# Kernel optimization log

Hardware: AMD Instinct MI355X
Metric: run time of the kernel (lower is better)

The kernel has to match this reference:

```python
import jax, jax.numpy as jnp
import numpy as np

# Dimensions implied by init_kwargs: dim=64, shape=(96,64,64), groups=8
DIM = 64          # in_planes = out_planes = conv channel dim (== spatial h == w)
CL = 96           # original channel dim c == attention sequence length
HS = 64           # spatial h (== DIM)
WS = 64           # spatial w (== DIM)
G = 8             # groups
GP = DIM // G     # group_planes = 8
EPS = 1e-5        # BatchNorm eps (inference mode with running stats)
B, T = 2, 16


def _bn(x, gamma, beta, mean, var, axis):
    """BatchNorm in inference mode along `axis`."""
    shp = [1] * x.ndim
    shp[axis] = -1
    return (x - mean.reshape(shp)) * jax.lax.rsqrt(var.reshape(shp) + EPS) * gamma.reshape(shp) + beta.reshape(shp)


def setup_inputs() -> dict:
    key = jax.random.key(0)
    ks = jax.random.split(key, 16)
    inp = {}
    inp["x"] = jax.random.normal(ks[0], (B, T, CL * HS * WS), jnp.float32)
    # qkv_transform: Conv1d(DIM, 2*DIM, kernel=1, bias=False) -> weight (2*DIM, DIM)
    inp["w_qkv"] = jax.random.normal(ks[1], (2 * DIM, DIM), jnp.float32) * np.float32(1.0 / np.sqrt(DIM))
    def bn_params(i, n):
        return (jnp.abs(jax.random.normal(ks[i], (n,), jnp.float32)) * 0.1 + 1.0,
                jax.random.normal(ks[i + 1], (n,), jnp.float32) * 0.1,
                jax.random.normal(ks[i + 2], (n,), jnp.float32) * 0.1,
                jnp.abs(jax.random.normal(ks[i + 3], (n,), jnp.float32)) * 0.1 + 1.0)
    (inp["qkv_gamma"], inp["qkv_beta"], inp["qkv_mean"], inp["qkv_var"]) = bn_params(2, 2 * DIM)
    (inp["sim_gamma"], inp["sim_beta"], inp["sim_mean"], inp["sim_var"]) = bn_params(6, G)
    (inp["out_gamma"], inp["out_beta"], inp["out_mean"], inp["out_var"]) = bn_params(10, DIM)
    return inp


def reference(x, w_qkv, qkv_gamma, qkv_beta, qkv_mean, qkv_var,
              sim_gamma, sim_beta, sim_mean, sim_var,
              out_gamma, out_beta, out_mean, out_var):
    b, t, F = x.shape
    NT = b * t
    xt = x.reshape(NT, CL, HS, WS)              # (NT, c, h, w)
    xt = jnp.transpose(xt, (0, 2, 3, 1))        # permute(0,2,3,1): (NT, h, w, c)
    xf = xt.reshape(NT * HS, WS, CL)            # view(NT*W, H, C): conv batch, channels=WS(=dim), len=c
    # 1x1 Conv1d + BN over channel dim
    qkv = jnp.einsum('oi,bil->bol', w_qkv, xf)  # (B2, 2*DIM, c)
    qkv = _bn(qkv, qkv_gamma, qkv_beta, qkv_mean, qkv_var, axis=1)
    qkv = qkv.reshape(NT * HS, G, 2 * GP, CL)
    q = qkv[:, :, : GP // 2]                    # (B2, G, GP//2, c)
    k = qkv[:, :, GP // 2: GP]                  # (B2, G, GP//2, c)
    v = qkv[:, :, GP:]                          # (B2, G, GP, c)
    qk = jnp.einsum('bgci,bgcj->bgij', q, k)    # (B2, G, c, c)
    qk = _bn(qk, sim_gamma, sim_beta, sim_mean, sim_var, axis=1)
    sim = jax.nn.softmax(qk, axis=3)
    sv = jnp.einsum('bgij,bgcj->bgci', sim, v)  # (B2, G, GP, c)
    sv = sv.reshape(NT * HS, DIM, CL)
    out = _bn(sv, out_gamma, out_beta, out_mean, out_var, axis=1)
    out = out.reshape(NT, HS, DIM, CL)          # (NT, W, out_planes, C); sum over size-1 dim is identity
    out = jnp.transpose(out, (0, 3, 2, 1))      # permute(0,3,2,1): (NT, c, dim, h) == (NT, c, h, w)
    return out.reshape(b, t, F)
```

## Files before the change

### kernel.cpp

```cpp
#include <hip/hip_runtime.h>

#define EPS 1e-5f
#define LOG2E 1.4426950408889634f

typedef short v8s __attribute__((ext_vector_type(8)));
typedef float v4f __attribute__((ext_vector_type(4)));

__device__ inline unsigned cvt_pk_bf16(float a, float b) {
    unsigned r;
    asm("v_cvt_pk_bf16_f32 %0, %1, %2" : "=v"(r) : "v"(a), "v"(b));
    return r;
}
__device__ inline unsigned short f2bf(float f) {
    return (unsigned short)cvt_pk_bf16(f, f);
}
__device__ inline float bf2f(unsigned short u) {
    union { unsigned u; float f; } v; v.u = (unsigned)u << 16;
    return v.f;
}

template<bool DIRECT>
__global__ __launch_bounds__(256, 3) void attn_kernel(
    const float* __restrict__ x,
    const float* __restrict__ w,
    const float* __restrict__ qkv_gamma, const float* __restrict__ qkv_beta,
    const float* __restrict__ qkv_mean,  const float* __restrict__ qkv_var,
    const float* __restrict__ sim_gamma, const float* __restrict__ sim_beta,
    const float* __restrict__ sim_mean,  const float* __restrict__ sim_var,
    const float* __restrict__ out_gamma, const float* __restrict__ out_beta,
    const float* __restrict__ out_mean,  const float* __restrict__ out_var,
    float* __restrict__ dst)
{
    __shared__ __align__(16) unsigned char smem[32256];
    unsigned short (*Qb)[96]  = (unsigned short(*)[96])smem;
    float (*Kf)[96]           = (float(*)[96])(smem + 6144);
    unsigned short (*Vb)[104] = (unsigned short(*)[104])(smem + 18432);
    unsigned short (*Xb)[72]  = (unsigned short(*)[72])smem;
    unsigned short (*Wb)[72]  = (unsigned short(*)[72])(smem + 13824);

    const int tid  = threadIdx.x;
    const int lane = tid & 63;
    const int wid  = tid >> 6;
    const int quad = lane >> 4;
    const int b  = blockIdx.x;
    const int nt = b >> 6;
    const int hs = b & 63;

    const float* xb = x + (size_t)nt * 393216 + (size_t)hs * 64;
    const float4* x4 = reinterpret_cast<const float4*>(xb);
    const float4* w4 = reinterpret_cast<const float4*>(w);

    #pragma unroll
    for (int it = 0; it < 6; ++it) {
        int idx = tid + it * 256;
        int cl = idx >> 4, v = idx & 15;
        float4 val = x4[cl * 1024 + v];
        unsigned* dx = (unsigned*)&Xb[cl][v * 4];
        dx[0] = cvt_pk_bf16(val.x, val.y);
        dx[1] = cvt_pk_bf16(val.z, val.w);
    }
    #pragma unroll
    for (int it = 0; it < 8; ++it) {
        int idx = tid + it * 256;
        int r = idx >> 4, v = idx & 15;
        float4 val = w4[r * 16 + v];
        unsigned* dw = (unsigned*)&Wb[r][v * 4];
        dw[0] = cvt_pk_bf16(val.x, val.y);
        dw[1] = cvt_pk_bf16(val.z, val.w);
    }
    __syncthreads();

    v4f acc1[2][6];
    #pragma unroll
    for (int mi = 0; mi < 2; ++mi)
        #pragma unroll
        for (int ni = 0; ni < 6; ++ni) acc1[mi][ni] = (v4f)(0.f);

    #pragma unroll
    for (int kt = 0; kt < 2; ++kt) {
        v8s a0 = *reinterpret_cast<const v8s*>(&Wb[(wid * 2 + 0) * 16 + (lane & 15)][kt * 32 + quad * 8]);
        v8s a1 = *reinterpret_cast<const v8s*>(&Wb[(wid * 2 + 1) * 16 + (lane & 15)][kt * 32 + quad * 8]);
        #pragma unroll
        for (int ni = 0; ni < 6; ++ni) {
            v8s bfr = *reinterpret_cast<const v8s*>(&Xb[ni * 16 + (lane & 15)][kt * 32 + quad * 8]);
            acc1[0][ni] = __builtin_amdgcn_mfma_f32_16x16x32_bf16(a0, bfr, acc1[0][ni], 0, 0, 0);
            acc1[1][ni] = __builtin_amdgcn_mfma_f32_16x16x32_bf16(a1, bfr, acc1[1][ni], 0, 0, 0);
        }
    }
    __syncthreads();

    #pragma unroll
    for (int mi = 0; mi < 2; ++mi) {
        const int mt = wid * 2 + mi;
        const float sA = sim_gamma[mt] * rsqrtf(sim_var[mt] + EPS) * LOG2E;
        #pragma unroll
        for (int reg = 0; reg < 4; ++reg) {
            int o = mt * 16 + quad * 4 + reg;
            int r = o & 15;
            float sc = qkv_gamma[o] * rsqrtf(qkv_var[o] + EPS);
            float mb = qkv_beta[o] - qkv_mean[o] * sc;
            if (r < 4) { sc *= sA; mb *= sA; }
            if (r < 4) {
                #pragma unroll
                for (int ni = 0; ni < 6; ++ni)
                    Qb[mt * 4 + r][ni * 16 + (lane & 15)] = f2bf(acc1[mi][ni][reg] * sc + mb);
            } else if (r < 8) {
                #pragma unroll
                for (int ni = 0; ni < 6; ++ni)
                    Kf[mt * 4 + (r - 4)][ni * 16 + (lane & 15)] = acc1[mi][ni][reg] * sc + mb;
            } else {
                #pragma unroll
                for (int ni = 0; ni < 6; ++ni)
                    Vb[mt * 8 + (r - 8)][ni * 16 + (lane & 15)] = f2bf(acc1[mi][ni][reg] * sc + mb);
            }
        }
    }

    const int r15 = lane & 15;

    for (int gi = 0; gi < 2; ++gi) {
        const int g = wid * 2 + gi;

        float qv[4][6];
        #pragma unroll
        for (int c = 0; c < 4; ++c)
            #pragma unroll
            for (int mt = 0; mt < 6; ++mt)
                qv[c][mt] = bf2f(Qb[g * 4 + c][mt * 16 + r15]);

        v4f acc[6];
        v4f rs4[6];
        #pragma unroll
        for (int mt = 0; mt < 6; ++mt) { acc[mt] = (v4f)(0.f); rs4[mt] = (v4f)(0.f); }

        const float* kbase = &Kf[g * 4][quad * 8];
        const unsigned short* vbase = &Vb[g * 8 + (lane & 7)][quad * 8];

        #pragma unroll
        for (int kt = 0; kt < 3; ++kt) {
            v4f kA[4], kB[4];
            #pragma unroll
            for (int c = 0; c < 4; ++c) {
                kA[c] = *reinterpret_cast<const v4f*>(kbase + c * 96 + kt * 32);
                kB[c] = *reinterpret_cast<const v4f*>(kbase + c * 96 + kt * 32 + 4);
            }
            v8s vf = *reinterpret_cast<const v8s*>(vbase + kt * 32);

            #pragma unroll
            for (int mt = 0; mt < 6; ++mt) {
                v4f sA = (v4f)(qv[0][mt]) * kA[0];
                v4f sB = (v4f)(qv[0][mt]) * kB[0];
                #pragma unroll
                for (int c = 1; c < 4; ++c) {
                    sA += (v4f)(qv[c][mt]) * kA[c];
                    sB += (v4f)(qv[c][mt]) * kB[c];
                }
                v4f eA, eB;
                #pragma unroll
                for (int jj = 0; jj < 4; ++jj) {
                    eA[jj] = __builtin_amdgcn_exp2f(sA[jj]);
                    eB[jj] = __builtin_amdgcn_exp2f(sB[jj]);
                }
                rs4[mt] += eA + eB;
                union { unsigned u[4]; v8s v; } pf;
                pf.u[0] = cvt_pk_bf16(eA[0], eA[1]);
                pf.u[1] = cvt_pk_bf16(eA[2], eA[3]);
                pf.u[2] = cvt_pk_bf16(eB[0], eB[1]);
                pf.u[3] = cvt_pk_bf16(eB[2], eB[3]);
                acc[mt] = __builtin_amdgcn_mfma_f32_16x16x32_bf16(pf.v, vf, acc[mt], 0, 0, 0);
            }
        }

        float zr[6];
        #pragma unroll
        for (int mt = 0; mt < 6; ++mt) {
            float t = (rs4[mt][0] + rs4[mt][1]) + (rs4[mt][2] + rs4[mt][3]);
            t += __shfl_xor(t, 16);
            t += __shfl_xor(t, 32);
            zr[mt] = __builtin_amdgcn_rcpf(t);
        }

        const int dd = g * 8 + (r15 & 7);
        float osc = out_gamma[dd] * rsqrtf(out_var[dd] + EPS);
        float ob  = out_beta[dd] - out_mean[dd] * osc;

        #pragma unroll
        for (int mt = 0; mt < 6; ++mt) {
            float zz[4];
            #pragma unroll
            for (int reg = 0; reg < 4; ++reg)
                zz[reg] = __shfl(zr[mt], quad * 4 + reg);
            if (r15 < 8) {
                float4 o4;
                o4.x = acc[mt][0] * (zz[0] * osc) + ob;
                o4.y = acc[mt][1] * (zz[1] * osc) + ob;
                o4.z = acc[mt][2] * (zz[2] * osc) + ob;
                o4.w = acc[mt][3] * (zz[3] * osc) + ob;
                if (DIRECT) {
                    const size_t base = (size_t)nt * 393216 + (size_t)dd * 64 + hs;
                    dst[base + (size_t)(mt * 16 + quad * 4 + 0) * 4096] = o4.x;
                    dst[base + (size_t)(mt * 16 + quad * 4 + 1) * 4096] = o4.y;
                    dst[base + (size_t)(mt * 16 + quad * 4 + 2) * 4096] = o4.z;
                    dst[base + (size_t)(mt * 16 + quad * 4 + 3) * 4096] = o4.w;
                } else {
                    reinterpret_cast<float4*>(dst)[(size_t)b * 1536 + dd * 24 + mt * 4 + quad] = o4;
                }
            }
        }
    }
}

__global__ __launch_bounds__(256) void transpose_kernel(const float* __restrict__ ws,
                                                        float* __restrict__ out)
{
    __shared__ float tile[64][97];
    const int blk = blockIdx.x;
    const int nt = blk >> 6, D = blk & 63;
    const float4* ws4 = reinterpret_cast<const float4*>(ws);
    v4f* out4 = reinterpret_cast<v4f*>(out);

    #pragma unroll
    for (int it = 0; it < 6; ++it) {
        int idx = threadIdx.x + it * 256;
        int hsr = idx / 24, c4 = idx - hsr * 24;
        float4 v = ws4[(size_t)nt * 98304 + (size_t)hsr * 1536 + D * 24 + c4];
        tile[hsr][c4 * 4 + 0] = v.x;
        tile[hsr][c4 * 4 + 1] = v.y;
        tile[hsr][c4 * 4 + 2] = v.z;
        tile[hsr][c4 * 4 + 3] = v.w;
    }
    __syncthreads();

    #pragma unroll
    for (int it = 0; it < 6; ++it) {
        int idx = threadIdx.x + it * 256;
        int cl = idx >> 4, h4 = idx & 15;
        v4f v;
        v[0] = tile[h4 * 4 + 0][cl];
        v[1] = tile[h4 * 4 + 1][cl];
        v[2] = tile[h4 * 4 + 2][cl];
        v[3] = tile[h4 * 4 + 3][cl];
        __builtin_nontemporal_store(v, &out4[(size_t)nt * 98304 + (size_t)cl * 1024 + D * 16 + h4]);
    }
}

extern "C" void kernel_launch(void* const* d_in, const int* in_sizes, int n_in,
                              void* d_out, int out_size, void* d_ws, size_t ws_size,
                              hipStream_t stream) {
    const float* x         = (const float*)d_in[0];
    const float* w_qkv     = (const float*)d_in[1];
    const float* qkv_gamma = (const float*)d_in[2];
    const float* qkv_beta  = (const float*)d_in[3];
    const float* qkv_mean  = (const float*)d_in[4];
    const float* qkv_var   = (const float*)d_in[5];
    const float* sim_gamma = (const float*)d_in[6];
    const float* sim_beta  = (const float*)d_in[7];
    const float* sim_mean  = (const float*)d_in[8];
    const float* sim_var   = (const float*)d_in[9];
    const float* out_gamma = (const float*)d_in[10];
    const float* out_beta  = (const float*)d_in[11];
    const float* out_mean  = (const float*)d_in[12];
    const float* out_var   = (const float*)d_in[13];
    float* out = (float*)d_out;

    const size_t ws_need = (size_t)2048 * 6144 * sizeof(float);

    if (ws_size >= ws_need) {
        float* wsb = (float*)d_ws;
        attn_kernel<false><<<2048, 256, 0, stream>>>(
            x, w_qkv, qkv_gamma, qkv_beta, qkv_mean, qkv_var,
            sim_gamma, sim_beta, sim_mean, sim_var,
            out_gamma, out_beta, out_mean, out_var, wsb);
        transpose_kernel<<<2048, 256, 0, stream>>>(wsb, out);
    } else {
        attn_kernel<true><<<2048, 256, 0, stream>>>(
            x, w_qkv, qkv_gamma, qkv_beta, qkv_mean, qkv_var,
            sim_gamma, sim_beta, sim_mean, sim_var,
            out_gamma, out_beta, out_mean, out_var, out);
    }
}
```

Baseline: 169.9 us.

## Drop transpose pass and remap blocks per XCD for direct scattered stores

Removes the workspace-plus-transpose two-kernel path and always writes output directly from the attention kernel with strided scalar stores. Block indices are remapped so that the blocks on each XCD cover contiguous halves of hs for the same nt. That way the scattered 4-byte stores from neighbouring hs values land in the same cache lines inside one XCD's L2. This saves a full workspace round-trip and a kernel launch, at the risk of poorly coalesced stores.

```diff
diff --git a/kernel.cpp b/kernel.cpp
--- a/kernel.cpp
+++ b/kernel.cpp
@@ -19,7 +19,6 @@
     return v.f;
 }
 
-template<bool DIRECT>
 __global__ __launch_bounds__(256, 3) void attn_kernel(
     const float* __restrict__ x,
     const float* __restrict__ w,
@@ -42,9 +41,15 @@
     const int lane = tid & 63;
     const int wid  = tid >> 6;
     const int quad = lane >> 4;
-    const int b  = blockIdx.x;
-    const int nt = b >> 6;
-    const int hs = b & 63;
+
+    const int bid = blockIdx.x;
+    const int xcd = bid & 7;
+    const int ixc = bid >> 3;
+    const int con = ixc >> 5;
+    const int wch = ixc & 31;
+    const int gch = con * 8 + xcd;
+    const int nt  = gch >> 1;
+    const int hs  = ((gch & 1) << 5) + wch;
 
     const float* xb = x + (size_t)nt * 393216 + (size_t)hs * 64;
     const float4* x4 = reinterpret_cast<const float4*>(xb);
@@ -196,51 +201,13 @@
                 o4.y = acc[mt][1] * (zz[1] * osc) + ob;
                 o4.z = acc[mt][2] * (zz[2] * osc) + ob;
                 o4.w = acc[mt][3] * (zz[3] * osc) + ob;
-                if (DIRECT) {
-                    const size_t base = (size_t)nt * 393216 + (size_t)dd * 64 + hs;
-                    dst[base + (size_t)(mt * 16 + quad * 4 + 0) * 4096] = o4.x;
-                    dst[base + (size_t)(mt * 16 + quad * 4 + 1) * 4096] = o4.y;
-                    dst[base + (size_t)(mt * 16 + quad * 4 + 2) * 4096] = o4.z;
-                    dst[base + (size_t)(mt * 16 + quad * 4 + 3) * 4096] = o4.w;
-                } else {
-                    reinterpret_cast<float4*>(dst)[(size_t)b * 1536 + dd * 24 + mt * 4 + quad] = o4;
-                }
-            }
-        }
-    }
-}
-
-__global__ __launch_bounds__(256) void transpose_kernel(const float* __restrict__ ws,
-                                                        float* __restrict__ out)
-{
-    __shared__ float tile[64][97];
-    const int blk = blockIdx.x;
-    const int nt = blk >> 6, D = blk & 63;
-    const float4* ws4 = reinterpret_cast<const float4*>(ws);
-    v4f* out4 = reinterpret_cast<v4f*>(out);
-
-    #pragma unroll
-    for (int it = 0; it < 6; ++it) {
-        int idx = threadIdx.x + it * 256;
-        int hsr = idx / 24, c4 = idx - hsr * 24;
-        float4 v = ws4[(size_t)nt * 98304 + (size_t)hsr * 1536 + D * 24 + c4];
-        tile[hsr][c4 * 4 + 0] = v.x;
-        tile[hsr][c4 * 4 + 1] = v.y;
-        tile[hsr][c4 * 4 + 2] = v.z;
-        tile[hsr][c4 * 4 + 3] = v.w;
-    }
-    __syncthreads();
-
-    #pragma unroll
-    for (int it = 0; it < 6; ++it) {
-        int idx = threadIdx.x + it * 256;
-        int cl = idx >> 4, h4 = idx & 15;
-        v4f v;
-        v[0] = tile[h4 * 4 + 0][cl];
-        v[1] = tile[h4 * 4 + 1][cl];
-        v[2] = tile[h4 * 4 + 2][cl];
-        v[3] = tile[h4 * 4 + 3][cl];
-        __builtin_nontemporal_store(v, &out4[(size_t)nt * 98304 + (size_t)cl * 1024 + D * 16 + h4]);
+                const size_t base = (size_t)nt * 393216 + (size_t)dd * 64 + hs;
+                dst[base + (size_t)(mt * 16 + quad * 4 + 0) * 4096] = o4.x;
+                dst[base + (size_t)(mt * 16 + quad * 4 + 1) * 4096] = o4.y;
+                dst[base + (size_t)(mt * 16 + quad * 4 + 2) * 4096] = o4.z;
+                dst[base + (size_t)(mt * 16 + quad * 4 + 3) * 4096] = o4.w;
+            }
+        }
     }
 }
 
@@ -263,19 +230,8 @@
     const float* out_var   = (const float*)d_in[13];
     float* out = (float*)d_out;
 
-    const size_t ws_need = (size_t)2048 * 6144 * sizeof(float);
-
-    if (ws_size >= ws_need) {
-        float* wsb = (float*)d_ws;
-        attn_kernel<false><<<2048, 256, 0, stream>>>(
-            x, w_qkv, qkv_gamma, qkv_beta, qkv_mean, qkv_var,
-            sim_gamma, sim_beta, sim_mean, sim_var,
-            out_gamma, out_beta, out_mean, out_var, wsb);
-        transpose_kernel<<<2048, 256, 0, stream>>>(wsb, out);
-    } else {
-        attn_kernel<true><<<2048, 256, 0, stream>>>(
-            x, w_qkv, qkv_gamma, qkv_beta, qkv_mean, qkv_var,
-            sim_gamma, sim_beta, sim_mean, sim_var,
-            out_gamma, out_beta, out_mean, out_var, out);
-    }
-}
+    attn_kernel<<<2048, 256, 0, stream>>>(
+        x, w_qkv, qkv_gamma, qkv_beta, qkv_mean, qkv_var,
+        sim_gamma, sim_beta, sim_mean, sim_var,
+        out_gamma, out_beta, out_mean, out_var, out);
+}
```

Result: slower. 180.0 us (+6.0%).
